# Optimization experiments

Measured on AMD Instinct MI355X. Metric: run time of the kernel, lower is better.

The kernel has to match this reference:

```python
import jax, jax.numpy as jnp
import numpy as np

TAU = 30.0
EPS = 1e-5

def layernorm(x, gamma, beta):
    mu = jnp.mean(x, axis=-1, keepdims=True)
    var = jnp.var(x, axis=-1, keepdims=True)
    return (x - mu) * jax.lax.rsqrt(var + EPS) * gamma + beta

def setup_inputs() -> dict:
    key = jax.random.key(0)
    ks = jax.random.split(key, 10)
    B, L, D, H, E = 2, 2048, 768, 12, 64
    x = jax.random.normal(ks[0], (B, L, D), dtype=jnp.float32)
    attention_mask = jnp.ones((B, L), dtype=jnp.int32)
    # stacked per-head projection weights, each head: (d_head, d_model)
    WQ = jax.random.normal(ks[1], (H, E, D), dtype=jnp.float32)
    WK = jax.random.normal(ks[2], (H, E, D), dtype=jnp.float32)
    WV = jax.random.normal(ks[3], (H, E, D), dtype=jnp.float32)
    gamma1 = jnp.ones((D,), jnp.float32); beta1 = jnp.zeros((D,), jnp.float32)
    gamma2 = jnp.ones((D,), jnp.float32); beta2 = jnp.zeros((D,), jnp.float32)
    W_O = jax.random.normal(ks[4], (D, D), dtype=jnp.float32)
    W_up = jax.random.normal(ks[5], (D, H * D), dtype=jnp.float32) * 0.02
    b_up = jnp.zeros((H * D,), jnp.float32)
    W_down = jax.random.normal(ks[6], (H * D, D), dtype=jnp.float32) * 0.02
    b_down = jnp.zeros((D,), jnp.float32)
    return {"x": x, "attention_mask": attention_mask, "WQ": WQ, "WK": WK, "WV": WV,
            "gamma1": gamma1, "beta1": beta1, "gamma2": gamma2, "beta2": beta2,
            "W_O": W_O, "W_up": W_up, "b_up": b_up, "W_down": W_down, "b_down": b_down}

def reference(x, attention_mask, WQ, WK, WV, gamma1, beta1, gamma2, beta2,
              W_O, W_up, b_up, W_down, b_down):
    B, L, D = x.shape
    E = WQ.shape[1]
    u = layernorm(x, gamma1, beta1)
    # per-head projections: (B, H, L, E)
    Q = jnp.einsum('bld,hed->bhle', u, WQ)
    K = jnp.einsum('bld,hed->bhle', u, WK)
    V = jnp.einsum('bld,hed->bhle', u, WV)
    S = jnp.einsum('bhle,bhme->bhlm', Q, K) / jnp.sqrt(jnp.float32(E))
    S = TAU * jnp.tanh(S)  # mode == 'tanh-clipped'
    causal = jnp.triu(jnp.ones((L, L), dtype=bool), k=1)  # True above diagonal
    S = jnp.where(causal, -jnp.inf, S)
    pad = (attention_mask == 0)[:, None, None, :]  # (B,1,1,L) key mask
    S = jnp.where(pad, -jnp.inf, S)
    A = jax.nn.softmax(S, axis=-1)
    O = jnp.einsum('bhlm,bhme->bhle', A, V)  # (B,H,L,E)
    heads_cat = O.transpose(0, 2, 1, 3).reshape(B, L, -1)  # (B,L,H*E)
    attn = heads_cat @ W_O.T
    z1 = x + attn
    v1 = layernorm(z1, gamma2, beta2)
    v3 = jax.nn.gelu(v1 @ W_up + b_up, approximate=False)
    z2 = z1 + v3 @ W_down + b_down
    return z2
```

## Files before the change

### kernel.cpp

```cpp
#include <hip/hip_runtime.h>
#include <stdint.h>

typedef __attribute__((ext_vector_type(8))) short bf16x8;
typedef __attribute__((ext_vector_type(4))) float f32x4;
typedef __attribute__((ext_vector_type(4))) unsigned short us4;
typedef unsigned short ushort;
typedef unsigned int uint;

#define MFMA16(a,b,c) __builtin_amdgcn_mfma_f32_16x16x32_bf16((a),(b),(c),0,0,0)

__device__ __forceinline__ ushort f2bf(float f){
  uint u = __builtin_bit_cast(uint, f);
  return (ushort)((u + 0x7fffu + ((u>>16)&1u)) >> 16);
}
__device__ __forceinline__ float bf2f(ushort h){
  return __builtin_bit_cast(float, ((uint)h)<<16);
}
__device__ __forceinline__ void gll16(const void* g, void* l){
  __builtin_amdgcn_global_load_lds((const __attribute__((address_space(1))) void*)g,
                                   (__attribute__((address_space(3))) void*)l, 16, 0, 0);
}

template<bool SPLIT, int BK>
__device__ __forceinline__ void gemm_core(
    const char* __restrict__ Ah, const char* __restrict__ Al,
    const char* __restrict__ Bh, const char* __restrict__ Bl,
    int K, int lda, int ldb, int m0, int n0,
    f32x4 acc[4][4], char* sAh, char* sAl, char* sBh, char* sBl)
{
  constexpr int ROWB = BK*2;
  constexpr int CHUNKS = 128*ROWB/1024;
  constexpr int XM = ((ROWB/16)-1) & 7;
  const int tid = threadIdx.x;
  const int wave = tid>>6, lane = tid&63;
  const int l15 = lane&15, l4 = lane>>4;
  const int wr = (wave>>1)*64, wc = (wave&1)*64;
  const int nsteps = K / BK;
  for (int kt = 0; kt < nsteps; ++kt) {
    const int kb0 = kt*ROWB;
    for (int c = wave; c < CHUNKS; c += 4) {
      const int p = (c<<10) + (lane<<4);
      const int row = p / ROWB;
      const int gk = (p % ROWB) ^ ((row & XM)<<4);
      gll16(Ah + (size_t)(m0+row)*lda + kb0 + gk, sAh + (c<<10));
      gll16(Bh + (size_t)(n0+row)*ldb + kb0 + gk, sBh + (c<<10));
      if constexpr (SPLIT) {
        gll16(Al + (size_t)(m0+row)*lda + kb0 + gk, sAl + (c<<10));
        gll16(Bl + (size_t)(n0+row)*ldb + kb0 + gk, sBl + (c<<10));
      }
    }
    __syncthreads();
    #pragma unroll
    for (int ks = 0; ks < BK/32; ++ks) {
      bf16x8 ah[4], bh_[4], al[4], bl[4];
      #pragma unroll
      for (int i = 0; i < 4; ++i) {
        const int ar = wr + i*16 + l15;
        const int ao = ar*ROWB + ((ks*64 + l4*16) ^ ((ar & XM)<<4));
        ah[i] = *(const bf16x8*)(sAh + ao);
        const int br = wc + i*16 + l15;
        const int bo = br*ROWB + ((ks*64 + l4*16) ^ ((br & XM)<<4));
        bh_[i] = *(const bf16x8*)(sBh + bo);
        if constexpr (SPLIT) {
          al[i] = *(const bf16x8*)(sAl + ao);
          bl[i] = *(const bf16x8*)(sBl + bo);
        }
      }
      #pragma unroll
      for (int mi = 0; mi < 4; ++mi) {
        #pragma unroll
        for (int ni = 0; ni < 4; ++ni) {
          acc[mi][ni] = MFMA16(ah[mi], bh_[ni], acc[mi][ni]);
          if constexpr (SPLIT) {
            acc[mi][ni] = MFMA16(ah[mi], bl[ni], acc[mi][ni]);
            acc[mi][ni] = MFMA16(al[mi], bh_[ni], acc[mi][ni]);
          }
        }
      }
    }
    __syncthreads();
  }
}

__global__ __launch_bounds__(256) void k_prep(
    const float* __restrict__ wq, const float* __restrict__ wk,
    const float* __restrict__ wv, const float* __restrict__ wo,
    ushort* qh, ushort* ql_, ushort* kh, ushort* kl_, ushort* vb, ushort* ob)
{
  int i = blockIdx.x*256 + threadIdx.x;
  if (i >= 589824) return;
  float a = wq[i]; ushort h = f2bf(a); qh[i]=h; ql_[i]=f2bf(a - bf2f(h));
  float b = wk[i]; h = f2bf(b); kh[i]=h; kl_[i]=f2bf(b - bf2f(h));
  vb[i] = f2bf(wv[i]); ob[i] = f2bf(wo[i]);
}

__global__ __launch_bounds__(256) void k_transpose(
    const float* __restrict__ in, ushort* __restrict__ out, int R, int C)
{
  __shared__ float t[32][33];
  const int bx = blockIdx.x*32, by = blockIdx.y*32;
  const int tx = threadIdx.x & 31, ty = threadIdx.x >> 5;
  #pragma unroll
  for (int i = 0; i < 4; ++i)
    t[ty + i*8][tx] = in[(size_t)(by + ty + i*8)*C + bx + tx];
  __syncthreads();
  #pragma unroll
  for (int i = 0; i < 4; ++i)
    out[(size_t)(bx + ty + i*8)*R + by + tx] = f2bf(t[tx][ty + i*8]);
}

__global__ __launch_bounds__(256) void k_ln(
    const float* __restrict__ in, const float* __restrict__ g, const float* __restrict__ be,
    ushort* __restrict__ oh, ushort* __restrict__ ol)
{
  const int row = blockIdx.x, t = threadIdx.x;
  const float* r = in + (size_t)row*768;
  float v0 = r[t], v1 = r[t+256], v2 = r[t+512];
  float s = v0+v1+v2;
  float q = v0*v0 + v1*v1 + v2*v2;
  #pragma unroll
  for (int m = 32; m; m >>= 1) { s += __shfl_xor(s, m); q += __shfl_xor(q, m); }
  __shared__ float ss[4], sq[4];
  const int wave = t>>6, lane = t&63;
  if (!lane) { ss[wave] = s; sq[wave] = q; }
  __syncthreads();
  s = ss[0]+ss[1]+ss[2]+ss[3];
  q = sq[0]+sq[1]+sq[2]+sq[3];
  const float mu = s*(1.f/768.f);
  const float var = q*(1.f/768.f) - mu*mu;
  const float inv = rsqrtf(var + 1e-5f);
  const float vv[3] = {v0, v1, v2};
  #pragma unroll
  for (int i = 0; i < 3; ++i) {
    const int idx = t + i*256;
    const float u = (vv[i]-mu)*inv*g[idx] + be[idx];
    const ushort hi = f2bf(u);
    oh[(size_t)row*768 + idx] = hi;
    if (ol) ol[(size_t)row*768 + idx] = f2bf(u - bf2f(hi));
  }
}

__global__ __launch_bounds__(256) void k_qkv(
    const ushort* __restrict__ uh, const ushort* __restrict__ ul,
    const ushort* __restrict__ wqh, const ushort* __restrict__ wql,
    const ushort* __restrict__ wkh, const ushort* __restrict__ wkl,
    const ushort* __restrict__ wvb,
    ushort* __restrict__ Qh, ushort* __restrict__ Ql,
    ushort* __restrict__ Kh, ushort* __restrict__ Kl,
    ushort* __restrict__ Vt)
{
  __shared__ char sA[8192], sA2[8192], sB[8192], sB2[8192];
  const int z = blockIdx.z;
  const int m0 = blockIdx.x*128, n0 = blockIdx.y*128;
  f32x4 acc[4][4] = {};
  if (z == 0)
    gemm_core<true,32>((const char*)uh, (const char*)ul, (const char*)wqh, (const char*)wql,
                       768, 1536, 1536, m0, n0, acc, sA, sA2, sB, sB2);
  else if (z == 1)
    gemm_core<true,32>((const char*)uh, (const char*)ul, (const char*)wkh, (const char*)wkl,
                       768, 1536, 1536, m0, n0, acc, sA, sA2, sB, sB2);
  else
    gemm_core<false,32>((const char*)uh, nullptr, (const char*)wvb, nullptr,
                        768, 1536, 1536, m0, n0, acc, sA, sA2, sB, sB2);

  const int tid = threadIdx.x, wave = tid>>6, lane = tid&63;
  const int l15 = lane&15, l4 = lane>>4;
  const int wr = (wave>>1)*64, wc = (wave&1)*64;
  if (z < 2) {
    ushort* __restrict__ Oh = z ? Kh : Qh;
    ushort* __restrict__ Ol = z ? Kl : Ql;
    #pragma unroll
    for (int mi = 0; mi < 4; ++mi) {
      #pragma unroll
      for (int ni = 0; ni < 4; ++ni) {
        const int he = n0 + wc + ni*16 + l15;
        const int h = he>>6, e = he&63;
        #pragma unroll
        for (int r = 0; r < 4; ++r) {
          const int n = m0 + wr + mi*16 + l4*4 + r;
          const int b = n>>11, l = n&2047;
          const size_t dst = ((size_t)((b*12+h)*2048 + l))*64 + e;
          const float c = acc[mi][ni][r];
          const ushort hi = f2bf(c);
          Oh[dst] = hi;
          Ol[dst] = f2bf(c - bf2f(hi));
        }
      }
    }
  } else {
    #pragma unroll
    for (int mi = 0; mi < 4; ++mi) {
      #pragma unroll
      for (int ni = 0; ni < 4; ++ni) {
        const int he = n0 + wc + ni*16 + l15;
        const int h = he>>6, e = he&63;
        const int n = m0 + wr + mi*16 + l4*4;
        const int b = n>>11, l = n&2047;
        us4 v;
        #pragma unroll
        for (int r = 0; r < 4; ++r) v[r] = f2bf(acc[mi][ni][r]);
        *(us4*)(Vt + ((size_t)((b*12+h)*64 + e))*2048 + l) = v;
      }
    }
  }
}

__global__ __launch_bounds__(256) void k_attn(
    const ushort* __restrict__ Qh, const ushort* __restrict__ Ql,
    const ushort* __restrict__ Kh, const ushort* __restrict__ Kl,
    const ushort* __restrict__ Vt, const int* __restrict__ am,
    ushort* __restrict__ Oc)
{
  __shared__ char sKh[8192], sKl[8192], sV[8192];
  __shared__ char sP[4][2048];
  const int qt = gridDim.x - 1 - blockIdx.x;
  const int bh = blockIdx.y;
  const int b = bh / 12, h = bh - b*12;
  const int tid = threadIdx.x, wave = tid>>6, lane = tid&63;
  const int l15 = lane&15, l4 = lane>>4;

  const size_t qoff = ((size_t)bh*2048 + qt*64 + wave*16 + l15)*64 + l4*8;
  const bf16x8 q_h0 = *(const bf16x8*)(Qh + qoff);
  const bf16x8 q_h1 = *(const bf16x8*)(Qh + qoff + 32);
  const bf16x8 q_l0 = *(const bf16x8*)(Ql + qoff);
  const bf16x8 q_l1 = *(const bf16x8*)(Ql + qoff + 32);

  f32x4 oacc[4] = {};
  float dsum[4] = {0.f, 0.f, 0.f, 0.f};
  const char* Kh_t = (const char*)(Kh + (size_t)bh*2048*64);
  const char* Kl_t = (const char*)(Kl + (size_t)bh*2048*64);
  const char* Vt_b = (const char*)(Vt + (size_t)bh*64*2048);

  for (int kt = 0; kt <= qt; ++kt) {
    for (int c = wave; c < 24; c += 4) {
      const int p = ((c&7)<<10) + (lane<<4);
      const int row = p >> 7;
      const int gkb = (p & 127) ^ ((row&7)<<4);
      const char* gsrc; char* lbase;
      if (c < 8)       { gsrc = Kh_t + (size_t)(kt*64+row)*128 + gkb; lbase = sKh + ((c&7)<<10); }
      else if (c < 16) { gsrc = Kl_t + (size_t)(kt*64+row)*128 + gkb; lbase = sKl + ((c&7)<<10); }
      else             { gsrc = Vt_b + (size_t)row*4096 + kt*128 + gkb; lbase = sV + ((c&7)<<10); }
      gll16(gsrc, lbase);
    }
    __syncthreads();

    f32x4 s[4] = {};
    #pragma unroll
    for (int ks = 0; ks < 2; ++ks) {
      bf16x8 kbh[4], kbl[4];
      #pragma unroll
      for (int nt = 0; nt < 4; ++nt) {
        const int key = nt*16 + l15;
        const int byte = key*128 + ((ks*64 + l4*16) ^ ((key&7)<<4));
        kbh[nt] = *(const bf16x8*)(sKh + byte);
        kbl[nt] = *(const bf16x8*)(sKl + byte);
      }
      const bf16x8 qh_ = ks ? q_h1 : q_h0;
      const bf16x8 ql_ = ks ? q_l1 : q_l0;
      #pragma unroll
      for (int nt = 0; nt < 4; ++nt) {
        s[nt] = MFMA16(qh_, kbh[nt], s[nt]);
        s[nt] = MFMA16(qh_, kbl[nt], s[nt]);
        s[nt] = MFMA16(ql_, kbh[nt], s[nt]);
      }
    }

    const bool diag = (kt == qt);
    #pragma unroll
    for (int nt = 0; nt < 4; ++nt) {
      const int key_g = kt*64 + nt*16 + l15;
      const float mv = (float)am[b*2048 + key_g];
      #pragma unroll
      for (int r = 0; r < 4; ++r) {
        const float sv = s[nt][r]*0.125f;
        float p = __expf(-60.f/(1.f + __expf(2.f*sv))) * mv;
        if (diag && key_g > qt*64 + wave*16 + l4*4 + r) p = 0.f;
        dsum[r] += p;
        const int qi = l4*4 + r;
        const int byte = qi*128 + ((nt*32 + l15*2) ^ ((qi&7)<<4));
        *(ushort*)(sP[wave] + byte) = f2bf(p);
      }
    }

    #pragma unroll
    for (int ks = 0; ks < 2; ++ks) {
      const int abyte = l15*128 + ((ks*64 + l4*16) ^ ((l15&7)<<4));
      const bf16x8 pa = *(const bf16x8*)(sP[wave] + abyte);
      #pragma unroll
      for (int et = 0; et < 4; ++et) {
        const int e_l = et*16 + l15;
        const int vbyte = e_l*128 + ((ks*64 + l4*16) ^ ((e_l&7)<<4));
        const bf16x8 vb = *(const bf16x8*)(sV + vbyte);
        oacc[et] = MFMA16(pa, vb, oacc[et]);
      }
    }
    __syncthreads();
  }

  #pragma unroll
  for (int r = 0; r < 4; ++r) {
    float d = dsum[r];
    d += __shfl_xor(d, 1); d += __shfl_xor(d, 2);
    d += __shfl_xor(d, 4); d += __shfl_xor(d, 8);
    dsum[r] = 1.f/d;
  }
  #pragma unroll
  for (int et = 0; et < 4; ++et) {
    #pragma unroll
    for (int r = 0; r < 4; ++r) {
      const int q_g = qt*64 + wave*16 + l4*4 + r;
      const size_t n = (size_t)b*2048 + q_g;
      const int he = h*64 + et*16 + l15;
      Oc[n*768 + he] = f2bf(oacc[et][r]*dsum[r]);
    }
  }
}

__global__ __launch_bounds__(256) void k_wo(
    const ushort* __restrict__ oc, const ushort* __restrict__ wob,
    float* __restrict__ z1)
{
  __shared__ char sA[16384], sB[16384];
  const int m0 = blockIdx.x*128, n0 = blockIdx.y*128;
  const int kz = blockIdx.z;
  f32x4 acc[4][4] = {};
  gemm_core<false,64>((const char*)oc + kz*768, nullptr, (const char*)wob + kz*768, nullptr,
                      384, 1536, 1536, m0, n0, acc, sA, nullptr, sB, nullptr);
  const int tid = threadIdx.x, wave = tid>>6, lane = tid&63;
  const int l15 = lane&15, l4 = lane>>4;
  const int wr = (wave>>1)*64, wc = (wave&1)*64;
  #pragma unroll
  for (int mi = 0; mi < 4; ++mi) {
    #pragma unroll
    for (int ni = 0; ni < 4; ++ni) {
      const int d = n0 + wc + ni*16 + l15;
      #pragma unroll
      for (int r = 0; r < 4; ++r) {
        const int n = m0 + wr + mi*16 + l4*4 + r;
        unsafeAtomicAdd(&z1[(size_t)n*768 + d], acc[mi][ni][r]);
      }
    }
  }
}

__global__ __launch_bounds__(256) void k_up(
    const ushort* __restrict__ v1, const ushort* __restrict__ wupT,
    const float* __restrict__ bup, ushort* __restrict__ v3)
{
  __shared__ char sA[16384], sB[16384];
  const int m0 = blockIdx.x*128, n0 = blockIdx.y*128;
  f32x4 acc[4][4] = {};
  gemm_core<false,64>((const char*)v1, nullptr, (const char*)wupT, nullptr,
                      768, 1536, 1536, m0, n0, acc, sA, nullptr, sB, nullptr);
  const int tid = threadIdx.x, wave = tid>>6, lane = tid&63;
  const int l15 = lane&15, l4 = lane>>4;
  const int wr = (wave>>1)*64, wc = (wave&1)*64;
  #pragma unroll
  for (int mi = 0; mi < 4; ++mi) {
    #pragma unroll
    for (int ni = 0; ni < 4; ++ni) {
      const int j = n0 + wc + ni*16 + l15;
      const float bj = bup[j];
      #pragma unroll
      for (int r = 0; r < 4; ++r) {
        const int n = m0 + wr + mi*16 + l4*4 + r;
        const float c = acc[mi][ni][r] + bj;
        const float ge = 0.5f*c*(1.f + erff(c*0.70710678118654752f));
        v3[(size_t)n*9216 + j] = f2bf(ge);
      }
    }
  }
}

__global__ __launch_bounds__(256) void k_oinit(
    const float* __restrict__ z1, const float* __restrict__ bdn, float* __restrict__ out)
{
  const int i = blockIdx.x*256 + threadIdx.x;
  const f32x4 z = *(const f32x4*)(z1 + (size_t)i*4);
  const int d = (i*4) % 768;
  f32x4 o;
  #pragma unroll
  for (int j = 0; j < 4; ++j) o[j] = z[j] + bdn[d+j];
  *(f32x4*)(out + (size_t)i*4) = o;
}

__global__ __launch_bounds__(256) void k_down(
    const ushort* __restrict__ v3, const ushort* __restrict__ wdnT,
    float* __restrict__ out)
{
  __shared__ char sA[16384], sB[16384];
  const int m0 = blockIdx.x*128, n0 = blockIdx.y*128;
  const int kz = blockIdx.z;
  f32x4 acc[4][4] = {};
  gemm_core<false,64>((const char*)v3 + kz*4608, nullptr, (const char*)wdnT + kz*4608, nullptr,
                      2304, 18432, 18432, m0, n0, acc, sA, nullptr, sB, nullptr);
  const int tid = threadIdx.x, wave = tid>>6, lane = tid&63;
  const int l15 = lane&15, l4 = lane>>4;
  const int wr = (wave>>1)*64, wc = (wave&1)*64;
  #pragma unroll
  for (int mi = 0; mi < 4; ++mi) {
    #pragma unroll
    for (int ni = 0; ni < 4; ++ni) {
      const int d = n0 + wc + ni*16 + l15;
      #pragma unroll
      for (int r = 0; r < 4; ++r) {
        const int n = m0 + wr + mi*16 + l4*4 + r;
        unsafeAtomicAdd(&out[(size_t)n*768 + d], acc[mi][ni][r]);
      }
    }
  }
}

extern "C" void kernel_launch(void* const* d_in, const int* in_sizes, int n_in,
                              void* d_out, int out_size, void* d_ws, size_t ws_size,
                              hipStream_t stream) {
  const float* x   = (const float*)d_in[0];
  const int*   am  = (const int*)d_in[1];
  const float* WQ  = (const float*)d_in[2];
  const float* WK  = (const float*)d_in[3];
  const float* WV  = (const float*)d_in[4];
  const float* g1  = (const float*)d_in[5];
  const float* b1  = (const float*)d_in[6];
  const float* g2  = (const float*)d_in[7];
  const float* b2  = (const float*)d_in[8];
  const float* WO  = (const float*)d_in[9];
  const float* Wup = (const float*)d_in[10];
  const float* bup = (const float*)d_in[11];
  const float* Wdn = (const float*)d_in[12];
  const float* bdn = (const float*)d_in[13];
  float* out = (float*)d_out;

  char* w = (char*)d_ws;
  ushort* wqh  = (ushort*)(w + 0);
  ushort* wql  = (ushort*)(w + 1179648);
  ushort* wkh  = (ushort*)(w + 2359296);
  ushort* wkl  = (ushort*)(w + 3538944);
  ushort* wvb  = (ushort*)(w + 4718592);
  ushort* wob  = (ushort*)(w + 5898240);
  ushort* wupT = (ushort*)(w + 7077888);
  ushort* wdnT = (ushort*)(w + 21233664);
  float*  z1   = (float*) (w + 35389440);
  ushort* v1h  = (ushort*)(w + 47972352);
  char*  pool  = w + 54263808;
  ushort* uh   = (ushort*)(pool + 0);
  ushort* ul   = (ushort*)(pool + 6291456);
  ushort* Qh_  = (ushort*)(pool + 12582912);
  ushort* Ql_  = (ushort*)(pool + 18874368);
  ushort* Kh_  = (ushort*)(pool + 25165824);
  ushort* Kl_  = (ushort*)(pool + 31457280);
  ushort* Vt_  = (ushort*)(pool + 37748736);
  ushort* oc   = (ushort*)(pool + 44040192);
  ushort* v3   = (ushort*)(pool + 0);
  const size_t NEED = 54263808u + 75497472u;
  if (ws_size < NEED) return;

  k_prep<<<2304, 256, 0, stream>>>(WQ, WK, WV, WO, wqh, wql, wkh, wkl, wvb, wob);
  k_transpose<<<dim3(288, 24), 256, 0, stream>>>(Wup, wupT, 768, 9216);
  k_transpose<<<dim3(24, 288), 256, 0, stream>>>(Wdn, wdnT, 9216, 768);
  k_ln<<<4096, 256, 0, stream>>>(x, g1, b1, uh, ul);
  k_qkv<<<dim3(32, 6, 3), 256, 0, stream>>>(uh, ul, wqh, wql, wkh, wkl, wvb,
                                            Qh_, Ql_, Kh_, Kl_, Vt_);
  k_attn<<<dim3(32, 24), 256, 0, stream>>>(Qh_, Ql_, Kh_, Kl_, Vt_, am, oc);
  hipMemcpyAsync(z1, x, 12582912, hipMemcpyDeviceToDevice, stream);
  k_wo<<<dim3(32, 6, 2), 256, 0, stream>>>(oc, wob, z1);
  k_ln<<<4096, 256, 0, stream>>>(z1, g2, b2, v1h, nullptr);
  k_up<<<dim3(32, 72), 256, 0, stream>>>(v1h, wupT, bup, v3);
  k_oinit<<<3072, 256, 0, stream>>>(z1, bdn, out);
  k_down<<<dim3(32, 6, 4), 256, 0, stream>>>(v3, wdnT, out);
}
```

Measured before the change: 530.9 us.

## Split causal attention over key chunks with atomic partial accumulation

Each query tile's key range is split into chunks of up to 8 key tiles, so the grid grows from 32 to 80 blocks per head. Blocks no longer run anywhere from 1 to 32 iterations, which evens out the causal load imbalance and raises occupancy. Partial numerators and denominators are added atomically into fp32 buffers, which are zeroed by memsets beforehand. A new normalization kernel then divides and writes the bf16 concatenated heads. The softmax exponent is also rewritten with a fast reciprocal. In exchange the change adds atomic traffic, two memsets, an extra kernel launch and non-deterministic summation order.

```diff
diff --git a/kernel.cpp b/kernel.cpp
--- a/kernel.cpp
+++ b/kernel.cpp
@@ -209,13 +209,21 @@
     const ushort* __restrict__ Qh, const ushort* __restrict__ Ql,
     const ushort* __restrict__ Kh, const ushort* __restrict__ Kl,
     const ushort* __restrict__ Vt, const int* __restrict__ am,
-    ushort* __restrict__ Oc)
+    float* __restrict__ Onum, float* __restrict__ Oden)
 {
   __shared__ char sKh[8192], sKl[8192], sV[8192];
   __shared__ char sP[4][2048];
-  const int qt = gridDim.x - 1 - blockIdx.x;
+  const int f = 79 - blockIdx.x;
+  int qt, c;
+  if (f < 8)       { qt = f;               c = 0; }
+  else if (f < 24) { int t = f-8;  qt = 8 +(t>>1); c = t&1; }
+  else if (f < 48) { int t = f-24; qt = 16+ t/3;   c = t - (qt-16)*3; }
+  else             { int t = f-48; qt = 24+(t>>2); c = t&3; }
+  const int kt0 = c*8;
+  const int kt1 = (kt0+8 < qt+1) ? kt0+8 : qt+1;
+
   const int bh = blockIdx.y;
-  const int b = bh / 12, h = bh - b*12;
+  const int b = bh / 12;
   const int tid = threadIdx.x, wave = tid>>6, lane = tid&63;
   const int l15 = lane&15, l4 = lane>>4;
 
@@ -231,15 +239,15 @@
   const char* Kl_t = (const char*)(Kl + (size_t)bh*2048*64);
   const char* Vt_b = (const char*)(Vt + (size_t)bh*64*2048);
 
-  for (int kt = 0; kt <= qt; ++kt) {
-    for (int c = wave; c < 24; c += 4) {
-      const int p = ((c&7)<<10) + (lane<<4);
+  for (int kt = kt0; kt < kt1; ++kt) {
+    for (int cc = wave; cc < 24; cc += 4) {
+      const int p = ((cc&7)<<10) + (lane<<4);
       const int row = p >> 7;
       const int gkb = (p & 127) ^ ((row&7)<<4);
       const char* gsrc; char* lbase;
-      if (c < 8)       { gsrc = Kh_t + (size_t)(kt*64+row)*128 + gkb; lbase = sKh + ((c&7)<<10); }
-      else if (c < 16) { gsrc = Kl_t + (size_t)(kt*64+row)*128 + gkb; lbase = sKl + ((c&7)<<10); }
-      else             { gsrc = Vt_b + (size_t)row*4096 + kt*128 + gkb; lbase = sV + ((c&7)<<10); }
+      if (cc < 8)       { gsrc = Kh_t + (size_t)(kt*64+row)*128 + gkb; lbase = sKh + ((cc&7)<<10); }
+      else if (cc < 16) { gsrc = Kl_t + (size_t)(kt*64+row)*128 + gkb; lbase = sKl + ((cc&7)<<10); }
+      else              { gsrc = Vt_b + (size_t)row*4096 + kt*128 + gkb; lbase = sV + ((cc&7)<<10); }
       gll16(gsrc, lbase);
     }
     __syncthreads();
@@ -272,8 +280,8 @@
       const float mv = (float)am[b*2048 + key_g];
       #pragma unroll
       for (int r = 0; r < 4; ++r) {
-        const float sv = s[nt][r]*0.125f;
-        float p = __expf(-60.f/(1.f + __expf(2.f*sv))) * mv;
+        const float es = __expf(0.25f*s[nt][r]);
+        float p = __expf(-60.f*__builtin_amdgcn_rcpf(1.f + es)) * mv;
         if (diag && key_g > qt*64 + wave*16 + l4*4 + r) p = 0.f;
         dsum[r] += p;
         const int qi = l4*4 + r;
@@ -302,18 +310,37 @@
     float d = dsum[r];
     d += __shfl_xor(d, 1); d += __shfl_xor(d, 2);
     d += __shfl_xor(d, 4); d += __shfl_xor(d, 8);
-    dsum[r] = 1.f/d;
+    dsum[r] = d;
+  }
+  const int qrow = qt*64 + wave*16 + l4*4;
+  if (l15 == 0) {
+    #pragma unroll
+    for (int r = 0; r < 4; ++r)
+      unsafeAtomicAdd(&Oden[bh*2048 + qrow + r], dsum[r]);
   }
   #pragma unroll
   for (int et = 0; et < 4; ++et) {
     #pragma unroll
-    for (int r = 0; r < 4; ++r) {
-      const int q_g = qt*64 + wave*16 + l4*4 + r;
-      const size_t n = (size_t)b*2048 + q_g;
-      const int he = h*64 + et*16 + l15;
-      Oc[n*768 + he] = f2bf(oacc[et][r]*dsum[r]);
-    }
-  }
+    for (int r = 0; r < 4; ++r)
+      unsafeAtomicAdd(&Onum[((size_t)bh*2048 + qrow + r)*64 + et*16 + l15], oacc[et][r]);
+  }
+}
+
+__global__ __launch_bounds__(256) void k_norm(
+    const float* __restrict__ Onum, const float* __restrict__ Oden,
+    ushort* __restrict__ Oc)
+{
+  const int i = blockIdx.x*256 + threadIdx.x;
+  const int row = i >> 4;
+  const int e0 = (i & 15)*4;
+  const int bh = row >> 11, l = row & 2047;
+  const int b = bh / 12, h = bh - b*12;
+  const float inv = 1.f / Oden[row];
+  const f32x4 v = *(const f32x4*)(Onum + (size_t)i*4);
+  us4 o;
+  #pragma unroll
+  for (int j = 0; j < 4; ++j) o[j] = f2bf(v[j]*inv);
+  *(us4*)(Oc + ((size_t)(b*2048 + l))*768 + h*64 + e0) = o;
 }
 
 __global__ __launch_bounds__(256) void k_wo(
@@ -450,6 +477,8 @@
   ushort* Kl_  = (ushort*)(pool + 31457280);
   ushort* Vt_  = (ushort*)(pool + 37748736);
   ushort* oc   = (ushort*)(pool + 44040192);
+  float* Onum  = (float*)(pool + 0);
+  float* Oden  = (float*)(pool + 50331648);
   ushort* v3   = (ushort*)(pool + 0);
   const size_t NEED = 54263808u + 75497472u;
   if (ws_size < NEED) return;
@@ -460,7 +489,10 @@
   k_ln<<<4096, 256, 0, stream>>>(x, g1, b1, uh, ul);
   k_qkv<<<dim3(32, 6, 3), 256, 0, stream>>>(uh, ul, wqh, wql, wkh, wkl, wvb,
                                             Qh_, Ql_, Kh_, Kl_, Vt_);
-  k_attn<<<dim3(32, 24), 256, 0, stream>>>(Qh_, Ql_, Kh_, Kl_, Vt_, am, oc);
+  hipMemsetAsync(Onum, 0, 12582912, stream);
+  hipMemsetAsync(Oden, 0, 196608, stream);
+  k_attn<<<dim3(80, 24), 256, 0, stream>>>(Qh_, Ql_, Kh_, Kl_, Vt_, am, Onum, Oden);
+  k_norm<<<3072, 256, 0, stream>>>(Onum, Oden, oc);
   hipMemcpyAsync(z1, x, 12582912, hipMemcpyDeviceToDevice, stream);
   k_wo<<<dim3(32, 6, 2), 256, 0, stream>>>(oc, wob, z1);
   k_ln<<<4096, 256, 0, stream>>>(z1, g2, b2, v1h, nullptr);
```

Measured after the change: 492.7 us. -7.2%, faster.
